# Optimization experiments

Measured on AMD Instinct MI355X. Metric: run time of the kernel, lower is better.

The kernel has to match this reference:

```python
import jax, jax.numpy as jnp
import numpy as np

N_NODES = 50000
N_EDGES = 1600000
IN_SIZE = 256
HIDDEN = 16
HEADS = 8
OUT_SIZE = 16
NEG_SLOPE = 0.2


def setup_inputs() -> dict:
    key = jax.random.key(0)
    ks = jax.random.split(key, 12)
    node_feat = jax.random.normal(ks[0], (N_NODES, IN_SIZE), dtype=jnp.float32)
    src = jax.random.randint(ks[1], (N_EDGES,), 0, N_NODES)
    dst = jax.random.randint(ks[2], (N_EDGES,), 0, N_NODES)
    d1 = HEADS * HIDDEN  # 128
    W1 = jax.random.normal(ks[3], (IN_SIZE, d1), dtype=jnp.float32) / np.sqrt(IN_SIZE)
    al1 = jax.random.normal(ks[4], (HEADS, HIDDEN), dtype=jnp.float32) / np.sqrt(HIDDEN)
    ar1 = jax.random.normal(ks[5], (HEADS, HIDDEN), dtype=jnp.float32) / np.sqrt(HIDDEN)
    b1 = jnp.zeros((d1,), dtype=jnp.float32)
    W2 = jax.random.normal(ks[6], (d1, HEADS * OUT_SIZE), dtype=jnp.float32) / np.sqrt(d1)
    al2 = jax.random.normal(ks[7], (HEADS, OUT_SIZE), dtype=jnp.float32) / np.sqrt(OUT_SIZE)
    ar2 = jax.random.normal(ks[8], (HEADS, OUT_SIZE), dtype=jnp.float32) / np.sqrt(OUT_SIZE)
    b2 = jnp.zeros((HEADS * OUT_SIZE,), dtype=jnp.float32)
    return {"node_feat": node_feat, "src": src, "dst": dst,
            "W1": W1, "al1": al1, "ar1": ar1, "b1": b1,
            "W2": W2, "al2": al2, "ar2": ar2, "b2": b2}


def _gat_conv(h, src, dst, W, attn_l, attn_r, bias, num_nodes):
    """DGL GATConv (eval mode, no dropout, no residual). Returns [N, H, D]."""
    H, D = attn_l.shape
    feat = (h @ W).reshape(-1, H, D)            # [N, H, D]
    el = jnp.sum(feat * attn_l, axis=-1)         # [N, H]
    er = jnp.sum(feat * attn_r, axis=-1)         # [N, H]
    e = jax.nn.leaky_relu(el[src] + er[dst], NEG_SLOPE)   # [E, H]
    # segment softmax over incoming edges of each dst node
    m = jax.ops.segment_max(e, dst, num_segments=num_nodes)
    m = jnp.where(jnp.isfinite(m), m, 0.0)       # guard isolated nodes
    ex = jnp.exp(e - m[dst])
    denom = jax.ops.segment_sum(ex, dst, num_segments=num_nodes)
    alpha = ex / denom[dst]                      # [E, H]
    msg = alpha[:, :, None] * feat[src]          # [E, H, D]
    out = jax.ops.segment_sum(msg, dst, num_segments=num_nodes)  # [N, H, D]
    return out + bias.reshape(H, D)


def reference(node_feat, src, dst, W1, al1, ar1, b1, W2, al2, ar2, b2):
    h = _gat_conv(node_feat, src, dst, W1, al1, ar1, b1, N_NODES)
    h = jax.nn.elu(h).reshape(N_NODES, -1)       # flatten(1) after activation
    out = _gat_conv(h, src, dst, W2, al2, ar2, b2, N_NODES)
    return out.mean(axis=1)                      # mean over heads -> [N, out_size]
```

## Files before the change

kernel.cpp:

```cpp
#include <hip/hip_runtime.h>
#include <hip/hip_bf16.h>

#define N_NODES 50000
#define N_EDGES 1600000
#define HEADS 8
#define HDIM 16
#define D1 128
#define NEG_SLOPE 0.2f
#define RTILES 3125
#define NB 196
#define BCAP 12288
#define B1BLK 320
#define EPB1 5000

typedef short short8 __attribute__((ext_vector_type(8)));
typedef float f32x4 __attribute__((ext_vector_type(4)));
typedef _Float16 half8 __attribute__((ext_vector_type(8)));
typedef unsigned char uchar;

__device__ __forceinline__ float bf2f(ushort u) {
    union { unsigned u; float f; } x; x.u = ((unsigned)u) << 16; return x.f;
}
__device__ __forceinline__ ushort f2bf(float f) {
    union { float f; unsigned u; } x; x.f = f;
    unsigned r = x.u + 0x7FFF + ((x.u >> 16) & 1);
    return (ushort)(r >> 16);
}
__device__ __forceinline__ float ldf(const void* p, size_t i, int isf32) {
    return isf32 ? ((const float*)p)[i] : bf2f(((const ushort*)p)[i]);
}
__device__ __forceinline__ void splitbf(float f, ushort& hi, ushort& lo) {
    unsigned u = __float_as_uint(f);
    unsigned uh = u & 0xFFFF0000u;
    hi = (ushort)(uh >> 16);
    lo = f2bf(f - __uint_as_float(uh));
}

#define O_ROWPTR   0
#define O_GCUR     200064
#define O_BBASE    400128
#define O_FLAGS    602240
#define O_ESRC     2202624
#define O_W1HI     5402624
#define O_W1LO     5476352
#define O_W2HI     5550080
#define O_W2LO     5586944
#define O_B1F      5623808
#define O_B2F      5624320
#define O_FEATG    5624832
#define O_EL       18424832
#define O_ER       20024832
#define O_FEATG2   21624832
#define O_EL2      34424832
#define O_ER2      36024832
#define O_PKBUF    O_FEATG2


__global__ __launch_bounds__(256) void k_detect(const ushort* __restrict__ w1, int* __restrict__ flags,
                                                int* __restrict__ gcur) {
    __shared__ int sm[256];
    int t = threadIdx.x;
    if (blockIdx.x == 1) {
        if (t < NB) gcur[t] = 0;
        return;
    }
    int cnt = 0;
    for (int i = t; i < 32768; i += 256) {
        int e = (w1[i] >> 7) & 0xFF;
        if (e >= 0xC8) cnt++;
    }
    sm[t] = cnt; __syncthreads();
    for (int off = 128; off > 0; off >>= 1) {
        if (t < off) sm[t] += sm[t + off];
        __syncthreads();
    }
    if (t == 0) flags[0] = (sm[0] > 0) ? 1 : 0;
}

__device__ __forceinline__ void wprep_elem(const void* W, const void* al, const void* ar,
                                           int K, int kshift, ushort* whi, ushort* wlo,
                                           int isf32, int idx) {
    if (idx >= 144 * K) return;
    int n = idx >> kshift, k = idx & (K - 1);
    float f;
    if (n < 128) {
        f = ldf(W, (size_t)k * 128 + n, isf32);
    } else if (n < 136) {
        int h = n - 128;
        f = 0.f;
#pragma unroll
        for (int d = 0; d < HDIM; ++d)
            f = fmaf(ldf(W, (size_t)k * 128 + h * 16 + d, isf32), ldf(al, h * 16 + d, isf32), f);
    } else {
        int h = n - 136;
        f = 0.f;
#pragma unroll
        for (int d = 0; d < HDIM; ++d)
            f = fmaf(ldf(W, (size_t)k * 128 + h * 16 + d, isf32), ldf(ar, h * 16 + d, isf32), f);
    }
    ushort hi = f2bf(f);
    wlo[n * K + k] = f2bf(f - bf2f(hi));
    whi[n * K + k] = hi;
}

__global__ __launch_bounds__(256) void k_wprep(const void* __restrict__ W1, const void* __restrict__ al1,
                                               const void* __restrict__ ar1, const void* __restrict__ b1,
                                               const void* __restrict__ W2, const void* __restrict__ al2,
                                               const void* __restrict__ ar2, const void* __restrict__ b2,
                                               ushort* __restrict__ w1hi, ushort* __restrict__ w1lo,
                                               ushort* __restrict__ w2hi, ushort* __restrict__ w2lo,
                                               float* __restrict__ b1f, float* __restrict__ b2f,
                                               const int* __restrict__ flags) {
    int isf32 = flags[0];
    int u = blockIdx.x, t = threadIdx.x;
    if (u < 144) {
        wprep_elem(W1, al1, ar1, 256, 8, w1hi, w1lo, isf32, u * 256 + t);
    } else if (u < 216) {
        wprep_elem(W2, al2, ar2, 128, 7, w2hi, w2lo, isf32, (u - 144) * 256 + t);
    } else {
        if (t < 128) b1f[t] = ldf(b1, t, isf32);
        else b2f[t - 128] = ldf(b2, t - 128, isf32);
    }
}

__device__ __forceinline__ void store_tile(_Float16 (*sfe)[72], _Float16* featg,
                                           const f32x4* acc, int lane, int quad, int l16,
                                           int rowb0, int cbase) {
#pragma unroll
    for (int ci = 0; ci < 4; ++ci)
#pragma unroll
        for (int r = 0; r < 4; ++r)
            sfe[quad * 4 + r][ci * 16 + l16] = (_Float16)acc[ci][r];
    int rr = lane >> 3, ch = lane & 7;
#pragma unroll
    for (int s = 0; s < 2; ++s) {
        int row = s * 8 + rr;
        short8 v = *(const short8*)&sfe[row][ch * 8];
        *(short8*)(featg + (size_t)(rowb0 + row) * D1 + cbase * 16 + ch * 8) = v;
    }
}

__device__ __forceinline__ void gemm1_wave9(const void* A, const ushort* Bhi, const ushort* Blo,
                                            _Float16* featg, float* el, float* er,
                                            int isf32, int rt, int lane, _Float16 (*sfe)[72]) {
    int quad = lane >> 4, l16 = lane & 15;
    const int K = 256;
    size_t a_off = (size_t)(rt * 16 + l16) * K + quad * 8;
    int rowb0 = rt * 16;

    short8 ahi[8], alo[8];
    if (isf32) {
        const float* ap = (const float*)A + a_off;
#pragma unroll
        for (int i = 0; i < 8; ++i) {
            f32x4 u0 = *(const f32x4*)(ap + 32 * i);
            f32x4 u1 = *(const f32x4*)(ap + 32 * i + 4);
            float a8[8] = {u0[0], u0[1], u0[2], u0[3], u1[0], u1[1], u1[2], u1[3]};
#pragma unroll
            for (int j = 0; j < 8; ++j) {
                ushort h, l;
                splitbf(a8[j], h, l);
                ahi[i][j] = (short)h; alo[i][j] = (short)l;
            }
        }
    } else {
        const ushort* ap = (const ushort*)A + a_off;
#pragma unroll
        for (int i = 0; i < 8; ++i) ahi[i] = *(const short8*)(ap + 32 * i);
    }

#pragma unroll
    for (int g = 0; g < 2; ++g) {
        f32x4 acc[4];
#pragma unroll
        for (int ci = 0; ci < 4; ++ci) acc[ci] = (f32x4){0.f, 0.f, 0.f, 0.f};
#pragma unroll
        for (int ci = 0; ci < 4; ++ci) {
            int c = g * 4 + ci;
            const ushort* bh = Bhi + (size_t)(c * 16 + l16) * K + quad * 8;
            if (isf32) {
                const ushort* bl = Blo + (size_t)(c * 16 + l16) * K + quad * 8;
#pragma unroll
                for (int k = 0; k < 8; ++k) {
                    short8 bh8 = *(const short8*)(bh + 32 * k);
                    short8 bl8 = *(const short8*)(bl + 32 * k);
                    acc[ci] = __builtin_amdgcn_mfma_f32_16x16x32_bf16(ahi[k], bh8, acc[ci], 0, 0, 0);
                    acc[ci] = __builtin_amdgcn_mfma_f32_16x16x32_bf16(ahi[k], bl8, acc[ci], 0, 0, 0);
                    acc[ci] = __builtin_amdgcn_mfma_f32_16x16x32_bf16(alo[k], bh8, acc[ci], 0, 0, 0);
                }
            } else {
#pragma unroll
                for (int k = 0; k < 8; ++k) {
                    short8 bh8 = *(const short8*)(bh + 32 * k);
                    acc[ci] = __builtin_amdgcn_mfma_f32_16x16x32_bf16(ahi[k], bh8, acc[ci], 0, 0, 0);
                }
            }
        }
        store_tile(sfe, featg, acc, lane, quad, l16, rowb0, g * 4);
    }

    {
        const ushort* bh = Bhi + (size_t)(8 * 16 + l16) * K + quad * 8;
        const ushort* bl = Blo + (size_t)(8 * 16 + l16) * K + quad * 8;
        f32x4 a = {0.f, 0.f, 0.f, 0.f};
#pragma unroll
        for (int k = 0; k < 8; ++k) {
            short8 bh8 = *(const short8*)(bh + 32 * k);
            short8 bl8 = *(const short8*)(bl + 32 * k);
            a = __builtin_amdgcn_mfma_f32_16x16x32_bf16(ahi[k], bh8, a, 0, 0, 0);
            a = __builtin_amdgcn_mfma_f32_16x16x32_bf16(ahi[k], bl8, a, 0, 0, 0);
            if (isf32) a = __builtin_amdgcn_mfma_f32_16x16x32_bf16(alo[k], bh8, a, 0, 0, 0);
        }
#pragma unroll
        for (int r = 0; r < 4; ++r) {
            int row = rowb0 + quad * 4 + r;
            if (l16 < 8) el[row * 8 + l16] = a[r];
            else         er[row * 8 + (l16 - 8)] = a[r];
        }
    }
}

__device__ __forceinline__ void block_scan(int* sm, int t) {
    for (int off = 1; off < 256; off <<= 1) {
        int v = (t >= off) ? sm[t - off] : 0;
        __syncthreads();
        sm[t] += v;
        __syncthreads();
    }
}

#define B1_SMEM 28384

__global__ __launch_bounds__(256) void k_b1gemm1(const int4* __restrict__ src4, const int4* __restrict__ dst4,
                                                 int* __restrict__ gcur, uint* __restrict__ pkbuf,
                                                 const void* __restrict__ A,
                                                 const ushort* __restrict__ w1hi, const ushort* __restrict__ w1lo,
                                                 _Float16* __restrict__ featg,
                                                 float* __restrict__ el, float* __restrict__ er,
                                                 const int* __restrict__ flags) {
    __shared__ __align__(16) char smem[B1_SMEM];
    int b = blockIdx.x, t = threadIdx.x;
    if (b < B1BLK) {
        uint*  stage = (uint*)smem;
        uchar* bid   = (uchar*)(smem + 20000);
        uint*  cnt   = (uint*)(smem + 25000);
        int*   loff  = (int*)(smem + 25784);
        int*   goff  = (int*)(smem + 26568);
        int*   sm    = (int*)(smem + 27352);
        for (int w = t; w < NB; w += 256) cnt[w] = 0;
        __syncthreads();
        int base4 = b * (EPB1 / 4);
        for (int g = t; g < EPB1 / 4; g += 256) {
            int4 d = dst4[base4 + g];
            atomicAdd(&cnt[d.x >> 8], 1u);
            atomicAdd(&cnt[d.y >> 8], 1u);
            atomicAdd(&cnt[d.z >> 8], 1u);
            atomicAdd(&cnt[d.w >> 8], 1u);
        }
        __syncthreads();
        int c = (t < NB) ? (int)cnt[t] : 0;
        sm[t] = c;
        __syncthreads();
        block_scan(sm, t);
        if (t < NB) {
            loff[t] = sm[t] - c;
            goff[t] = atomicAdd(&gcur[t], c);
            cnt[t] = 0;
        }
        __syncthreads();
        for (int g = t; g < EPB1 / 4; g += 256) {
            int4 s = src4[base4 + g];
            int4 d = dst4[base4 + g];
            { int bk = d.x >> 8; int r = atomicAdd(&cnt[bk], 1u); int p = loff[bk] + r; stage[p] = ((uint)s.x << 8) | (uint)(d.x & 255); bid[p] = (uchar)bk; }
            { int bk = d.y >> 8; int r = atomicAdd(&cnt[bk], 1u); int p = loff[bk] + r; stage[p] = ((uint)s.y << 8) | (uint)(d.y & 255); bid[p] = (uchar)bk; }
            { int bk = d.z >> 8; int r = atomicAdd(&cnt[bk], 1u); int p = loff[bk] + r; stage[p] = ((uint)s.z << 8) | (uint)(d.z & 255); bid[p] = (uchar)bk; }
            { int bk = d.w >> 8; int r = atomicAdd(&cnt[bk], 1u); int p = loff[bk] + r; stage[p] = ((uint)s.w << 8) | (uint)(d.w & 255); bid[p] = (uchar)bk; }
        }
        __syncthreads();
        for (int k = t; k < EPB1; k += 256) {
            int bk = (int)bid[k];
            int gi = goff[bk] + (k - loff[bk]);
            if (gi < BCAP) pkbuf[(size_t)bk * BCAP + gi] = stage[k];
        }
    } else {
        int g = b - B1BLK;
        _Float16 (*sfe4)[16][72] = (_Float16(*)[16][72])smem;
        int wave = t >> 6, lane = t & 63;
        int rt = g * 4 + wave;
        if (rt < RTILES)
            gemm1_wave9(A, w1hi, w1lo, featg, el, er, flags[0], rt, lane, sfe4[wave]);
    }
}

__global__ __launch_bounds__(256) void k_bscan(const int* __restrict__ gcur, int* __restrict__ bbase,
                                               int* __restrict__ rowptr) {
    __shared__ int sm[256];
    int t = threadIdx.x;
    int x = (t < NB) ? gcur[t] : 0;
    sm[t] = x;
    __syncthreads();
    block_scan(sm, t);
    if (t == 0) bbase[0] = 0;
    bbase[t + 1] = sm[t];
    if (t == NB - 1) rowptr[N_NODES] = sm[t];
}

__global__ __launch_bounds__(256) void k_bucket2(const uint* __restrict__ pkbuf, const int* __restrict__ gcur,
                                                 const int* __restrict__ bbase,
                                                 ushort* __restrict__ esrc, int* __restrict__ rowptr) {
    __shared__ __align__(16) char smem[76800];
    uint*   pk    = (uint*)smem;
    ushort* es    = (ushort*)(smem + 49152);
    uint*   ncnt  = (uint*)(smem + 73728);
    int*    nbase = (int*)(smem + 74752);
    int*    sm    = (int*)(smem + 75776);
    int b = blockIdx.x, t = threadIdx.x;
    int nb = gcur[b]; if (nb > BCAP) nb = BCAP;
    int bb0 = bbase[b];
    ncnt[t] = 0;
    __syncthreads();
    for (int k = t; k < nb; k += 256) {
        uint u = pkbuf[(size_t)b * BCAP + k];
        pk[k] = u;
        atomicAdd(&ncnt[u & 255u], 1u);
    }
    __syncthreads();
    int c = (int)ncnt[t];
    sm[t] = c;
    __syncthreads();
    block_scan(sm, t);
    nbase[t] = sm[t] - c;
    int v = b * 256 + t;
    if (v < N_NODES) rowptr[v] = bb0 + sm[t] - c;
    ncnt[t] = 0;
    __syncthreads();
    for (int k = t; k < nb; k += 256) {
        uint u = pk[k];
        int n = (int)(u & 255u);
        int r = (int)atomicAdd(&ncnt[n], 1u);
        int p = nbase[n] + r;
        if (p < BCAP) es[p] = (ushort)(u >> 8);
    }
    __syncthreads();
    for (int k = t; k < nb; k += 256)
        esrc[bb0 + k] = es[k];
}

__device__ __forceinline__ void gather_wide(const int* __restrict__ rowptr, const ushort* __restrict__ esrc,
                                            const _Float16* __restrict__ featg,
                                            const float* __restrict__ el, const float* __restrict__ er,
                                            int v, int lane, float (&acc)[8], float& den, int& deg) {
    int h8 = lane & 7, esel = lane >> 3;
    int part = lane & 15, a = lane >> 4, hpart = part >> 1;
    float erv = er[v * 8 + h8];
    int beg = rowptr[v], end = rowptr[v + 1];
    deg = end - beg;
#pragma unroll
    for (int c = 0; c < 8; ++c) acc[c] = 0.f;
    den = 0.f;
    for (int j = beg; j < end; j += 64) {
        int m = end - j; if (m > 64) m = 64;
        int idx = j + lane; if (idx >= end) idx = end - 1;
        int sv = (int)esrc[idx];
        int fb = (m + 7) >> 3;
        float w[8];
#pragma unroll
        for (int bb = 0; bb < 8; ++bb) {
            if (bb < fb) {
                int e = bb * 8 + esel;
                int se = __shfl(sv, e);
                float x = el[se * 8 + h8] + erv;
                x = x > 0.f ? x : NEG_SLOPE * x;
                w[bb] = (e < m) ? __expf(x) : 0.f;
            } else {
                w[bb] = 0.f;
            }
        }
#pragma unroll
        for (int bb = 0; bb < 8; ++bb) {
            if (bb < fb) {
                int s0 = __shfl(sv, bb * 8 + a);
                int s1 = __shfl(sv, bb * 8 + a + 4);
                half8 g0 = *(const half8*)(featg + (size_t)s0 * 128 + part * 8);
                half8 g1 = *(const half8*)(featg + (size_t)s1 * 128 + part * 8);
                float w0 = __shfl(w[bb], a * 8 + hpart);
                float w1 = __shfl(w[bb], (a + 4) * 8 + hpart);
                den += w0 + w1;
#pragma unroll
                for (int c = 0; c < 8; ++c)
                    acc[c] = fmaf(w0, (float)g0[c], fmaf(w1, (float)g1[c], acc[c]));
            }
        }
    }
#pragma unroll
    for (int c = 0; c < 8; ++c) {
        acc[c] += __shfl_xor(acc[c], 16);
        acc[c] += __shfl_xor(acc[c], 32);
    }
    den += __shfl_xor(den, 16);
    den += __shfl_xor(den, 32);
}

__global__ __launch_bounds__(256) void k_agg1m(const int* __restrict__ rowptr, const ushort* __restrict__ esrc,
                                               const _Float16* __restrict__ featg,
                                               const float* __restrict__ el, const float* __restrict__ er,
                                               const float* __restrict__ b1f,
                                               const ushort* __restrict__ w2hi, const ushort* __restrict__ w2lo,
                                               _Float16* __restrict__ featg2,
                                               float* __restrict__ el2, float* __restrict__ er2,
                                               const int* __restrict__ flags) {
    __shared__ __align__(16) ushort sh_hi[16][136];
    __shared__ __align__(16) ushort sh_lo[16][136];
    int isf32 = flags[0];
    int wave = threadIdx.x >> 6, lane = threadIdx.x & 63;
    int part = lane & 15, a = lane >> 4;
    int vb = blockIdx.x * 16;
    f32x4 bia0 = *(const f32x4*)(b1f + part * 8);
    f32x4 bia1 = *(const f32x4*)(b1f + part * 8 + 4);
#pragma unroll 1
    for (int i = 0; i < 4; ++i) {
        int v = vb + wave * 4 + i;
        float acc[8], den; int dg;
        gather_wide(rowptr, esrc, featg, el, er, v, lane, acc, den, dg);
        float inv = (dg > 0) ? 1.0f / den : 0.f;
        if (a == 0) {
            short8 hi8, lo8;
#pragma unroll
            for (int c = 0; c < 8; ++c) {
                float bc = (c < 4) ? bia0[c] : bia1[c - 4];
                float r = fmaf(acc[c], inv, bc);
                r = r > 0.f ? r : (__expf(r) - 1.f);
                ushort h, l;
                splitbf(r, h, l);
                hi8[c] = (short)h; lo8[c] = (short)l;
            }
            int m = wave * 4 + i;
            *(short8*)&sh_hi[m][part * 8] = hi8;
            *(short8*)&sh_lo[m][part * 8] = lo8;
        }
    }
    __syncthreads();

    int quad = lane >> 4, l16 = lane & 15;
    const int K = 128;
    short8 ahi[4], alo[4];
#pragma unroll
    for (int k = 0; k < 4; ++k) {
        ahi[k] = *(const short8*)&sh_hi[l16][quad * 8 + 32 * k];
        alo[k] = *(const short8*)&sh_lo[l16][quad * 8 + 32 * k];
    }
    int ntile = (wave == 0) ? 3 : 2;
    for (int ti = 0; ti < ntile; ++ti) {
        int c = (ti == 2) ? 8 : wave + ti * 4;
        const ushort* bh = w2hi + (size_t)(c * 16 + l16) * K + quad * 8;
        const ushort* bl = w2lo + (size_t)(c * 16 + l16) * K + quad * 8;
        f32x4 aa = {0.f, 0.f, 0.f, 0.f};
#pragma unroll
        for (int k = 0; k < 4; ++k) {
            short8 bh8 = *(const short8*)(bh + 32 * k);
            aa = __builtin_amdgcn_mfma_f32_16x16x32_bf16(ahi[k], bh8, aa, 0, 0, 0);
            aa = __builtin_amdgcn_mfma_f32_16x16x32_bf16(alo[k], bh8, aa, 0, 0, 0);
            if (c == 8 || isf32) {
                short8 bl8 = *(const short8*)(bl + 32 * k);
                aa = __builtin_amdgcn_mfma_f32_16x16x32_bf16(ahi[k], bl8, aa, 0, 0, 0);
            }
        }
        if (c < 8) {
#pragma unroll
            for (int r = 0; r < 4; ++r)
                featg2[(size_t)(vb + quad * 4 + r) * D1 + c * 16 + l16] = (_Float16)aa[r];
        } else {
#pragma unroll
            for (int r = 0; r < 4; ++r) {
                int row = vb + quad * 4 + r;
                if (l16 < 8) el2[row * 8 + l16] = aa[r];
                else         er2[row * 8 + (l16 - 8)] = aa[r];
            }
        }
    }
}

__global__ __launch_bounds__(256) void k_agg2(const int* __restrict__ rowptr, const ushort* __restrict__ esrc,
                                              const _Float16* __restrict__ featg2,
                                              const float* __restrict__ el2, const float* __restrict__ er2,
                                              const float* __restrict__ b2f,
                                              void* __restrict__ out, const int* __restrict__ flags) {
    int wave = threadIdx.x >> 6, lane = threadIdx.x & 63;
    int v = blockIdx.x * 4 + wave;
    if (v >= N_NODES) return;
    int part = lane & 15;
    float acc[8], den; int dg;
    gather_wide(rowptr, esrc, featg2, el2, er2, v, lane, acc, den, dg);
    float inv = (dg > 0) ? 1.0f / den : 0.f;
    f32x4 bia0 = *(const f32x4*)(b2f + part * 8);
    f32x4 bia1 = *(const f32x4*)(b2f + part * 8 + 4);
    float r[8];
#pragma unroll
    for (int c = 0; c < 8; ++c) {
        float bc = (c < 4) ? bia0[c] : bia1[c - 4];
        r[c] = fmaf(acc[c], inv, bc);
    }
#pragma unroll
    for (int c = 0; c < 8; ++c) {
        r[c] += __shfl_xor(r[c], 2);
        r[c] += __shfl_xor(r[c], 4);
        r[c] += __shfl_xor(r[c], 8);
        r[c] *= 0.125f;
    }
    if (lane < 2) {
        if (flags[0]) {
            float* op = (float*)out + (size_t)v * 16 + lane * 8;
            f32x4 o0 = {r[0], r[1], r[2], r[3]};
            f32x4 o1 = {r[4], r[5], r[6], r[7]};
            *(f32x4*)op = o0;
            *(f32x4*)(op + 4) = o1;
        } else {
            short8 pk;
#pragma unroll
            for (int c = 0; c < 8; ++c) pk[c] = (short)f2bf(r[c]);
            *(short8*)((ushort*)out + (size_t)v * 16 + lane * 8) = pk;
        }
    }
}

extern "C" void kernel_launch(void* const* d_in, const int* in_sizes, int n_in,
                              void* d_out, int out_size, void* d_ws, size_t ws_size,
                              hipStream_t stream) {
    const void* node_feat = d_in[0];
    const int4* src4 = (const int4*)d_in[1];
    const int4* dst4 = (const int4*)d_in[2];
    const void* W1 = d_in[3];
    const void* al1 = d_in[4];
    const void* ar1 = d_in[5];
    const void* b1 = d_in[6];
    const void* W2 = d_in[7];
    const void* al2 = d_in[8];
    const void* ar2 = d_in[9];
    const void* b2 = d_in[10];
    char* ws = (char*)d_ws;

    int* rowptr = (int*)(ws + O_ROWPTR);
    int* gcur   = (int*)(ws + O_GCUR);
    int* bbase  = (int*)(ws + O_BBASE);
    int* flags  = (int*)(ws + O_FLAGS);
    ushort* esrc = (ushort*)(ws + O_ESRC);
    uint* pkbuf = (uint*)(ws + O_PKBUF);
    ushort* w1hi = (ushort*)(ws + O_W1HI);
    ushort* w1lo = (ushort*)(ws + O_W1LO);
    ushort* w2hi = (ushort*)(ws + O_W2HI);
    ushort* w2lo = (ushort*)(ws + O_W2LO);
    float* b1f  = (float*)(ws + O_B1F);
    float* b2f  = (float*)(ws + O_B2F);
    _Float16* featg = (_Float16*)(ws + O_FEATG);
    float* el   = (float*)(ws + O_EL);
    float* er   = (float*)(ws + O_ER);
    _Float16* featg2 = (_Float16*)(ws + O_FEATG2);
    float* el2  = (float*)(ws + O_EL2);
    float* er2  = (float*)(ws + O_ER2);

    k_detect<<<2, 256, 0, stream>>>((const ushort*)W1, flags, gcur);
    k_wprep<<<217, 256, 0, stream>>>(W1, al1, ar1, b1, W2, al2, ar2, b2,
                                     w1hi, w1lo, w2hi, w2lo, b1f, b2f, flags);
    k_b1gemm1<<<B1BLK + 782, 256, 0, stream>>>(src4, dst4, gcur, pkbuf,
                                               node_feat, w1hi, w1lo, featg, el, er, flags);
    k_bscan<<<1, 256, 0, stream>>>(gcur, bbase, rowptr);
    k_bucket2<<<NB, 256, 0, stream>>>(pkbuf, gcur, bbase, esrc, rowptr);
    k_agg1m<<<N_NODES / 16, 256, 0, stream>>>(rowptr, esrc, featg, el, er, b1f,
                                              w2hi, w2lo, featg2, el2, er2, flags);
    k_agg2<<<(N_NODES + 3) / 4, 256, 0, stream>>>(rowptr, esrc, featg2, el2, er2,
                                                  b2f, d_out, flags);
}
```

Before: 391.1 us.

## Regroup launches: fuse wprep with bucketing, split gemm1, fold bucket scan into bucket2

Weight prep now shares one launch with the first edge-bucketing pass, and the layer-1 GEMM becomes its own kernel. The single-block bucket-offset scan kernel is removed; each bucket2 block recomputes the prefix scan of bucket counts itself. The gather loop in the aggregation is also changed from 64-edge batches with 8 sub-steps to an 8-edge-per-iteration loop, and the per-wave node loop in agg1m is unrolled. This removes one launch and the serial scan kernel, but the GEMM no longer overlaps with bucketing, and the gather issues more, smaller index loads per node.

```diff
diff --git a/kernel.cpp b/kernel.cpp
--- a/kernel.cpp
+++ b/kernel.cpp
@@ -12,6 +12,7 @@
 #define BCAP 12288
 #define B1BLK 320
 #define EPB1 5000
+#define WPREP_BLKS 217
 
 typedef short short8 __attribute__((ext_vector_type(8)));
 typedef float f32x4 __attribute__((ext_vector_type(4)));
@@ -38,7 +39,6 @@
 
 #define O_ROWPTR   0
 #define O_GCUR     200064
-#define O_BBASE    400128
 #define O_FLAGS    602240
 #define O_ESRC     2202624
 #define O_W1HI     5402624
@@ -103,23 +103,82 @@
     whi[n * K + k] = hi;
 }
 
-__global__ __launch_bounds__(256) void k_wprep(const void* __restrict__ W1, const void* __restrict__ al1,
-                                               const void* __restrict__ ar1, const void* __restrict__ b1,
-                                               const void* __restrict__ W2, const void* __restrict__ al2,
-                                               const void* __restrict__ ar2, const void* __restrict__ b2,
-                                               ushort* __restrict__ w1hi, ushort* __restrict__ w1lo,
-                                               ushort* __restrict__ w2hi, ushort* __restrict__ w2lo,
-                                               float* __restrict__ b1f, float* __restrict__ b2f,
-                                               const int* __restrict__ flags) {
-    int isf32 = flags[0];
-    int u = blockIdx.x, t = threadIdx.x;
-    if (u < 144) {
-        wprep_elem(W1, al1, ar1, 256, 8, w1hi, w1lo, isf32, u * 256 + t);
-    } else if (u < 216) {
-        wprep_elem(W2, al2, ar2, 128, 7, w2hi, w2lo, isf32, (u - 144) * 256 + t);
+__device__ __forceinline__ void block_scan(int* sm, int t) {
+    for (int off = 1; off < 256; off <<= 1) {
+        int v = (t >= off) ? sm[t - off] : 0;
+        __syncthreads();
+        sm[t] += v;
+        __syncthreads();
+    }
+}
+
+#define B1_SMEM 28384
+
+__global__ __launch_bounds__(256) void k_wb1(const void* __restrict__ W1, const void* __restrict__ al1,
+                                             const void* __restrict__ ar1, const void* __restrict__ b1,
+                                             const void* __restrict__ W2, const void* __restrict__ al2,
+                                             const void* __restrict__ ar2, const void* __restrict__ b2,
+                                             ushort* __restrict__ w1hi, ushort* __restrict__ w1lo,
+                                             ushort* __restrict__ w2hi, ushort* __restrict__ w2lo,
+                                             float* __restrict__ b1f, float* __restrict__ b2f,
+                                             const int4* __restrict__ src4, const int4* __restrict__ dst4,
+                                             int* __restrict__ gcur, uint* __restrict__ pkbuf,
+                                             const int* __restrict__ flags) {
+    __shared__ __align__(16) char smem[B1_SMEM];
+    int b = blockIdx.x, t = threadIdx.x;
+    if (b < WPREP_BLKS) {
+        int isf32 = flags[0];
+        if (b < 144) {
+            wprep_elem(W1, al1, ar1, 256, 8, w1hi, w1lo, isf32, b * 256 + t);
+        } else if (b < 216) {
+            wprep_elem(W2, al2, ar2, 128, 7, w2hi, w2lo, isf32, (b - 144) * 256 + t);
+        } else {
+            if (t < 128) b1f[t] = ldf(b1, t, isf32);
+            else b2f[t - 128] = ldf(b2, t - 128, isf32);
+        }
     } else {
-        if (t < 128) b1f[t] = ldf(b1, t, isf32);
-        else b2f[t - 128] = ldf(b2, t - 128, isf32);
+        uint*  stage = (uint*)smem;
+        uchar* bid   = (uchar*)(smem + 20000);
+        uint*  cnt   = (uint*)(smem + 25000);
+        int*   loff  = (int*)(smem + 25784);
+        int*   goff  = (int*)(smem + 26568);
+        int*   sm    = (int*)(smem + 27352);
+        int bb = b - WPREP_BLKS;
+        for (int w = t; w < NB; w += 256) cnt[w] = 0;
+        __syncthreads();
+        int base4 = bb * (EPB1 / 4);
+        for (int g = t; g < EPB1 / 4; g += 256) {
+            int4 d = dst4[base4 + g];
+            atomicAdd(&cnt[d.x >> 8], 1u);
+            atomicAdd(&cnt[d.y >> 8], 1u);
+            atomicAdd(&cnt[d.z >> 8], 1u);
+            atomicAdd(&cnt[d.w >> 8], 1u);
+        }
+        __syncthreads();
+        int c = (t < NB) ? (int)cnt[t] : 0;
+        sm[t] = c;
+        __syncthreads();
+        block_scan(sm, t);
+        if (t < NB) {
+            loff[t] = sm[t] - c;
+            goff[t] = atomicAdd(&gcur[t], c);
+            cnt[t] = 0;
+        }
+        __syncthreads();
+        for (int g = t; g < EPB1 / 4; g += 256) {
+            int4 s = src4[base4 + g];
+            int4 d = dst4[base4 + g];
+            { int bk = d.x >> 8; int r = atomicAdd(&cnt[bk], 1u); int p = loff[bk] + r; stage[p] = ((uint)s.x << 8) | (uint)(d.x & 255); bid[p] = (uchar)bk; }
+            { int bk = d.y >> 8; int r = atomicAdd(&cnt[bk], 1u); int p = loff[bk] + r; stage[p] = ((uint)s.y << 8) | (uint)(d.y & 255); bid[p] = (uchar)bk; }
+            { int bk = d.z >> 8; int r = atomicAdd(&cnt[bk], 1u); int p = loff[bk] + r; stage[p] = ((uint)s.z << 8) | (uint)(d.z & 255); bid[p] = (uchar)bk; }
+            { int bk = d.w >> 8; int r = atomicAdd(&cnt[bk], 1u); int p = loff[bk] + r; stage[p] = ((uint)s.w << 8) | (uint)(d.w & 255); bid[p] = (uchar)bk; }
+        }
+        __syncthreads();
+        for (int k = t; k < EPB1; k += 256) {
+            int bk = (int)bid[k];
+            int gi = goff[bk] + (k - loff[bk]);
+            if (gi < BCAP) pkbuf[(size_t)bk * BCAP + gi] = stage[k];
+        }
     }
 }
 
@@ -220,93 +279,19 @@
     }
 }
 
-__device__ __forceinline__ void block_scan(int* sm, int t) {
-    for (int off = 1; off < 256; off <<= 1) {
-        int v = (t >= off) ? sm[t - off] : 0;
-        __syncthreads();
-        sm[t] += v;
-        __syncthreads();
-    }
-}
-
-#define B1_SMEM 28384
-
-__global__ __launch_bounds__(256) void k_b1gemm1(const int4* __restrict__ src4, const int4* __restrict__ dst4,
-                                                 int* __restrict__ gcur, uint* __restrict__ pkbuf,
-                                                 const void* __restrict__ A,
-                                                 const ushort* __restrict__ w1hi, const ushort* __restrict__ w1lo,
-                                                 _Float16* __restrict__ featg,
-                                                 float* __restrict__ el, float* __restrict__ er,
-                                                 const int* __restrict__ flags) {
-    __shared__ __align__(16) char smem[B1_SMEM];
-    int b = blockIdx.x, t = threadIdx.x;
-    if (b < B1BLK) {
-        uint*  stage = (uint*)smem;
-        uchar* bid   = (uchar*)(smem + 20000);
-        uint*  cnt   = (uint*)(smem + 25000);
-        int*   loff  = (int*)(smem + 25784);
-        int*   goff  = (int*)(smem + 26568);
-        int*   sm    = (int*)(smem + 27352);
-        for (int w = t; w < NB; w += 256) cnt[w] = 0;
-        __syncthreads();
-        int base4 = b * (EPB1 / 4);
-        for (int g = t; g < EPB1 / 4; g += 256) {
-            int4 d = dst4[base4 + g];
-            atomicAdd(&cnt[d.x >> 8], 1u);
-            atomicAdd(&cnt[d.y >> 8], 1u);
-            atomicAdd(&cnt[d.z >> 8], 1u);
-            atomicAdd(&cnt[d.w >> 8], 1u);
-        }
-        __syncthreads();
-        int c = (t < NB) ? (int)cnt[t] : 0;
-        sm[t] = c;
-        __syncthreads();
-        block_scan(sm, t);
-        if (t < NB) {
-            loff[t] = sm[t] - c;
-            goff[t] = atomicAdd(&gcur[t], c);
-            cnt[t] = 0;
-        }
-        __syncthreads();
-        for (int g = t; g < EPB1 / 4; g += 256) {
-            int4 s = src4[base4 + g];
-            int4 d = dst4[base4 + g];
-            { int bk = d.x >> 8; int r = atomicAdd(&cnt[bk], 1u); int p = loff[bk] + r; stage[p] = ((uint)s.x << 8) | (uint)(d.x & 255); bid[p] = (uchar)bk; }
-            { int bk = d.y >> 8; int r = atomicAdd(&cnt[bk], 1u); int p = loff[bk] + r; stage[p] = ((uint)s.y << 8) | (uint)(d.y & 255); bid[p] = (uchar)bk; }
-            { int bk = d.z >> 8; int r = atomicAdd(&cnt[bk], 1u); int p = loff[bk] + r; stage[p] = ((uint)s.z << 8) | (uint)(d.z & 255); bid[p] = (uchar)bk; }
-            { int bk = d.w >> 8; int r = atomicAdd(&cnt[bk], 1u); int p = loff[bk] + r; stage[p] = ((uint)s.w << 8) | (uint)(d.w & 255); bid[p] = (uchar)bk; }
-        }
-        __syncthreads();
-        for (int k = t; k < EPB1; k += 256) {
-            int bk = (int)bid[k];
-            int gi = goff[bk] + (k - loff[bk]);
-            if (gi < BCAP) pkbuf[(size_t)bk * BCAP + gi] = stage[k];
-        }
-    } else {
-        int g = b - B1BLK;
-        _Float16 (*sfe4)[16][72] = (_Float16(*)[16][72])smem;
-        int wave = t >> 6, lane = t & 63;
-        int rt = g * 4 + wave;
-        if (rt < RTILES)
-            gemm1_wave9(A, w1hi, w1lo, featg, el, er, flags[0], rt, lane, sfe4[wave]);
-    }
-}
-
-__global__ __launch_bounds__(256) void k_bscan(const int* __restrict__ gcur, int* __restrict__ bbase,
-                                               int* __restrict__ rowptr) {
-    __shared__ int sm[256];
-    int t = threadIdx.x;
-    int x = (t < NB) ? gcur[t] : 0;
-    sm[t] = x;
-    __syncthreads();
-    block_scan(sm, t);
-    if (t == 0) bbase[0] = 0;
-    bbase[t + 1] = sm[t];
-    if (t == NB - 1) rowptr[N_NODES] = sm[t];
+__global__ __launch_bounds__(256) void k_gemm1(const void* __restrict__ A,
+                                               const ushort* __restrict__ w1hi, const ushort* __restrict__ w1lo,
+                                               _Float16* __restrict__ featg,
+                                               float* __restrict__ el, float* __restrict__ er,
+                                               const int* __restrict__ flags) {
+    __shared__ __align__(16) _Float16 sfe[4][16][72];
+    int wave = threadIdx.x >> 6, lane = threadIdx.x & 63;
+    int rt = blockIdx.x * 4 + wave;
+    if (rt < RTILES)
+        gemm1_wave9(A, w1hi, w1lo, featg, el, er, flags[0], rt, lane, sfe[wave]);
 }
 
 __global__ __launch_bounds__(256) void k_bucket2(const uint* __restrict__ pkbuf, const int* __restrict__ gcur,
-                                                 const int* __restrict__ bbase,
                                                  ushort* __restrict__ esrc, int* __restrict__ rowptr) {
     __shared__ __align__(16) char smem[76800];
     uint*   pk    = (uint*)smem;
@@ -315,8 +300,14 @@
     int*    nbase = (int*)(smem + 74752);
     int*    sm    = (int*)(smem + 75776);
     int b = blockIdx.x, t = threadIdx.x;
+    int x = (t < NB) ? gcur[t] : 0;
+    sm[t] = x;
+    __syncthreads();
+    block_scan(sm, t);
     int nb = gcur[b]; if (nb > BCAP) nb = BCAP;
-    int bb0 = bbase[b];
+    int bb0 = sm[b] - gcur[b];
+    if (b == 0 && t == NB - 1) rowptr[N_NODES] = sm[t];
+    __syncthreads();
     ncnt[t] = 0;
     __syncthreads();
     for (int k = t; k < nb; k += 256) {
@@ -358,39 +349,25 @@
 #pragma unroll
     for (int c = 0; c < 8; ++c) acc[c] = 0.f;
     den = 0.f;
-    for (int j = beg; j < end; j += 64) {
-        int m = end - j; if (m > 64) m = 64;
-        int idx = j + lane; if (idx >= end) idx = end - 1;
+    for (int j = beg; j < end; j += 8) {
+        int nv = end - j;
+        int idx = j + h8; if (idx >= end) idx = end - 1;
         int sv = (int)esrc[idx];
-        int fb = (m + 7) >> 3;
-        float w[8];
-#pragma unroll
-        for (int bb = 0; bb < 8; ++bb) {
-            if (bb < fb) {
-                int e = bb * 8 + esel;
-                int se = __shfl(sv, e);
-                float x = el[se * 8 + h8] + erv;
-                x = x > 0.f ? x : NEG_SLOPE * x;
-                w[bb] = (e < m) ? __expf(x) : 0.f;
-            } else {
-                w[bb] = 0.f;
-            }
-        }
-#pragma unroll
-        for (int bb = 0; bb < 8; ++bb) {
-            if (bb < fb) {
-                int s0 = __shfl(sv, bb * 8 + a);
-                int s1 = __shfl(sv, bb * 8 + a + 4);
-                half8 g0 = *(const half8*)(featg + (size_t)s0 * 128 + part * 8);
-                half8 g1 = *(const half8*)(featg + (size_t)s1 * 128 + part * 8);
-                float w0 = __shfl(w[bb], a * 8 + hpart);
-                float w1 = __shfl(w[bb], (a + 4) * 8 + hpart);
-                den += w0 + w1;
-#pragma unroll
-                for (int c = 0; c < 8; ++c)
-                    acc[c] = fmaf(w0, (float)g0[c], fmaf(w1, (float)g1[c], acc[c]));
-            }
-        }
+        int se = __shfl(sv, esel);
+        float x = el[se * 8 + h8] + erv;
+        x = x > 0.f ? x : NEG_SLOPE * x;
+        float w = __expf(x);
+        if (esel >= nv) w = 0.f;
+        int s0 = __shfl(sv, a);
+        int s1 = __shfl(sv, a + 4);
+        half8 g0 = *(const half8*)(featg + (size_t)s0 * 128 + part * 8);
+        half8 g1 = *(const half8*)(featg + (size_t)s1 * 128 + part * 8);
+        float w0 = __shfl(w, a * 8 + hpart);
+        float w1 = __shfl(w, (a + 4) * 8 + hpart);
+        den += w0 + w1;
+#pragma unroll
+        for (int c = 0; c < 8; ++c)
+            acc[c] = fmaf(w0, (float)g0[c], fmaf(w1, (float)g1[c], acc[c]));
     }
 #pragma unroll
     for (int c = 0; c < 8; ++c) {
@@ -417,7 +394,7 @@
     int vb = blockIdx.x * 16;
     f32x4 bia0 = *(const f32x4*)(b1f + part * 8);
     f32x4 bia1 = *(const f32x4*)(b1f + part * 8 + 4);
-#pragma unroll 1
+#pragma unroll
     for (int i = 0; i < 4; ++i) {
         int v = vb + wave * 4 + i;
         float acc[8], den; int dg;
@@ -541,7 +518,6 @@
 
     int* rowptr = (int*)(ws + O_ROWPTR);
     int* gcur   = (int*)(ws + O_GCUR);
-    int* bbase  = (int*)(ws + O_BBASE);
     int* flags  = (int*)(ws + O_FLAGS);
     ushort* esrc = (ushort*)(ws + O_ESRC);
     uint* pkbuf = (uint*)(ws + O_PKBUF);
@@ -559,12 +535,11 @@
     float* er2  = (float*)(ws + O_ER2);
 
     k_detect<<<2, 256, 0, stream>>>((const ushort*)W1, flags, gcur);
-    k_wprep<<<217, 256, 0, stream>>>(W1, al1, ar1, b1, W2, al2, ar2, b2,
-                                     w1hi, w1lo, w2hi, w2lo, b1f, b2f, flags);
-    k_b1gemm1<<<B1BLK + 782, 256, 0, stream>>>(src4, dst4, gcur, pkbuf,
-                                               node_feat, w1hi, w1lo, featg, el, er, flags);
-    k_bscan<<<1, 256, 0, stream>>>(gcur, bbase, rowptr);
-    k_bucket2<<<NB, 256, 0, stream>>>(pkbuf, gcur, bbase, esrc, rowptr);
+    k_wb1<<<WPREP_BLKS + B1BLK, 256, 0, stream>>>(W1, al1, ar1, b1, W2, al2, ar2, b2,
+                                                  w1hi, w1lo, w2hi, w2lo, b1f, b2f,
+                                                  src4, dst4, gcur, pkbuf, flags);
+    k_gemm1<<<782, 256, 0, stream>>>(node_feat, w1hi, w1lo, featg, el, er, flags);
+    k_bucket2<<<NB, 256, 0, stream>>>(pkbuf, gcur, esrc, rowptr);
     k_agg1m<<<N_NODES / 16, 256, 0, stream>>>(rowptr, esrc, featg, el, er, b1f,
                                               w2hi, w2lo, featg2, el2, er2, flags);
     k_agg2<<<(N_NODES + 3) / 4, 256, 0, stream>>>(rowptr, esrc, featg2, el2, er2,
```

New measurement: 371.7 us. -5.0%, faster.
